# Optimization experiments

Measured on AMD Instinct MI355X. Metric: run time of the kernel, lower is better.

Reference implementation:

```python
import jax, jax.numpy as jnp
import numpy as np

B, DIM, H, W = 8, 384, 64, 64
HEADS = 8
D = DIM // HEADS          # 48
D2 = D // 2               # 24
DU = D // 3 * 2           # 32 (ratio=3)


def setup_inputs() -> dict:
    key = jax.random.key(0)
    ks = jax.random.split(key, 12)
    s = lambda k, shape, scale=0.05: jax.random.normal(k, shape, jnp.float32) * scale
    return {
        "x": jax.random.normal(ks[0], (B, DIM, H, W), jnp.float32),
        "temperature": jnp.ones((HEADS, 1, 1), jnp.float32),
        "w_qkv": s(ks[1], (3 * DIM, DIM)),          # 1x1 conv, no bias
        "w_dw": s(ks[2], (3 * DIM, 1, 3, 3)),       # depthwise 3x3, groups=3*dim
        "w_proj": s(ks[3], (DIM, HEADS)),           # project_out 1x1
        "w_attn_r": s(ks[4], (1, D)),
        "w_v_r": s(ks[5], (D2, D)),
        "w_up1": s(ks[6], (DU, D2)),
        "b_up1": jnp.zeros((DU,), jnp.float32),
        "ln_w": jnp.ones((DU, HEADS, 1), jnp.float32),
        "ln_b": jnp.zeros((DU, HEADS, 1), jnp.float32),
        "w_up2": s(ks[7], (D, DU)),
        "b_up2": jnp.zeros((D,), jnp.float32),
        "w_attn_l": s(ks[8], (D2, D)),
        "w_v_l": s(ks[9], (D2, D)),
    }


def _qkv_attn(x, temperature, w_qkv, w_dw):
    # shared: qkv 1x1 conv -> depthwise 3x3 -> split, normalize, elementwise attn+softmax
    b, c, h, w = x.shape
    qkv = jnp.einsum('bchw,oc->bohw', x, w_qkv)
    qkv = jax.lax.conv_general_dilated(
        qkv, w_dw, (1, 1), 'SAME', feature_group_count=3 * c,
        dimension_numbers=('NCHW', 'OIHW', 'NCHW'))
    q, k, v = jnp.split(qkv, 3, axis=1)
    rs = lambda t: t.reshape(b, HEADS, D, h * w)  # b (head d) h w -> b head d (hw)
    q, k, v = rs(q), rs(k), rs(v)
    qn = q / jnp.maximum(jnp.linalg.norm(q, axis=-1, keepdims=True), 1e-12)
    kn = k / jnp.maximum(jnp.linalg.norm(k, axis=-1, keepdims=True), 1e-12)
    attn = jax.nn.softmax(qn * kn * temperature, axis=-1)  # [b, head, d, s]
    return attn, v


def _forward(x, temperature, w_qkv, w_dw, w_proj, w_attn_r, w_v_r,
             w_up1, b_up1, ln_w, ln_b, w_up2, b_up2, w_attn_l, w_v_l):
    b, c, h, w = x.shape
    attn, v = _qkv_attn(x, temperature, w_qkv, w_dw)

    # ---- spatial_pool (channel gating) ----
    input_x = jnp.einsum('bhds,od->bhos', v, w_v_r)                 # conv_v_right: [b,head,d2,s]
    cm = jax.nn.softmax(jnp.einsum('bhds,d->bhs', attn, w_attn_r[0]), axis=-1)  # conv_attn_right + softmax
    ctx = jnp.einsum('bhs,bhjs->bhj', cm, input_x)                  # [b,head,d2]
    ctx = ctx.transpose(0, 2, 1)[..., None]                         # [b, d2, head, 1]
    u = jnp.einsum('bchl,oc->bohl', ctx, w_up1) + b_up1[None, :, None, None]  # [b, DU, head, 1]
    mu = u.mean(axis=(1, 2, 3), keepdims=True)
    var = u.var(axis=(1, 2, 3), keepdims=True)
    u = (u - mu) / jnp.sqrt(var + 1e-5) * ln_w[None] + ln_b[None]   # LayerNorm([DU, 8, 1])
    u = jax.nn.relu(u)
    u = jnp.einsum('bchl,oc->bohl', u, w_up2) + b_up2[None, :, None, None]    # [b, D, head, 1]
    mask_ch = jax.nn.sigmoid(u).reshape(b, c, 1, 1)                 # view(b, head*D, 1, 1)
    out_channel = x * mask_ch

    # ---- channel_pool (spatial gating) ----
    g = jnp.einsum('bhds,od->bhos', attn, w_attn_l)                 # conv_attn_left: [b,head,d2,s]
    avg = jax.nn.softmax(g.mean(axis=-1), axis=-1)                  # avg-pool over s, softmax over d2
    theta = jnp.einsum('bhds,od->bhos', v, w_v_l)                   # conv_v_left: [b,head,d2,s]
    ctx2 = jnp.einsum('bhd,bhds->bhs', avg, theta)                  # matmul: [b,head,s]
    mask_sp = jax.nn.sigmoid(ctx2).reshape(b, HEADS, h, w)
    mask_sp = jnp.einsum('bchw,oc->bohw', mask_sp, w_proj)          # project_out
    out_spatial = x * mask_sp

    return out_spatial + out_channel


def reference(x, temperature, w_qkv, w_dw, w_proj, w_attn_r, w_v_r,
              w_up1, b_up1, ln_w, ln_b, w_up2, b_up2, w_attn_l, w_v_l):
    return _forward(x, temperature, w_qkv, w_dw, w_proj, w_attn_r, w_v_r,
                    w_up1, b_up1, ln_w, ln_b, w_up2, b_up2, w_attn_l, w_v_l)
```

## Files before the change

kernel.cpp:

```cpp
#include <hip/hip_runtime.h>
#include <math.h>


#define S4096 4096
#define C384  384
#define OC    1152

typedef unsigned short bfraw;
typedef unsigned int   u32;
typedef __attribute__((ext_vector_type(8))) short bf16x8;
typedef __attribute__((ext_vector_type(4))) float f32x4;

typedef __attribute__((address_space(3))) unsigned int lds_u32;
typedef const __attribute__((address_space(1))) unsigned int glb_u32;
__device__ __forceinline__ void gll16(const void* g, void* l) {
    __builtin_amdgcn_global_load_lds((glb_u32*)g, (lds_u32*)l, 16, 0, 0);
}

__device__ __forceinline__ bfraw f2bf(float f) {
    union { float f; u32 u; } c; c.f = f;
    u32 r = c.u + 0x7FFFu + ((c.u >> 16) & 1u);
    return (bfraw)(r >> 16);
}
__device__ __forceinline__ float bf2f(bfraw u) {
    union { u32 u; float f; } c; c.u = ((u32)u) << 16;
    return c.f;
}
__device__ __forceinline__ void unpack8(uint4 v, float* f) {
    f[0] = bf2f((bfraw)(v.x & 0xffff)); f[1] = bf2f((bfraw)(v.x >> 16));
    f[2] = bf2f((bfraw)(v.y & 0xffff)); f[3] = bf2f((bfraw)(v.y >> 16));
    f[4] = bf2f((bfraw)(v.z & 0xffff)); f[5] = bf2f((bfraw)(v.z >> 16));
    f[6] = bf2f((bfraw)(v.w & 0xffff)); f[7] = bf2f((bfraw)(v.w >> 16));
}
__device__ __forceinline__ uint4 pack8(const float* f) {
    union { bfraw us[8]; uint4 q; } p;
    #pragma unroll
    for (int i = 0; i < 8; i++) p.us[i] = f2bf(f[i]);
    return p.q;
}

__device__ __forceinline__ float blk_red(float v, float* s4, bool ismax) {
    #pragma unroll
    for (int off = 32; off; off >>= 1) {
        float o = __shfl_down(v, off, 64);
        v = ismax ? fmaxf(v, o) : (v + o);
    }
    __syncthreads();
    if ((threadIdx.x & 63) == 0) s4[threadIdx.x >> 6] = v;
    __syncthreads();
    return ismax ? fmaxf(fmaxf(s4[0], s4[1]), fmaxf(s4[2], s4[3]))
                 : ((s4[0] + s4[1]) + (s4[2] + s4[3]));
}

__global__ __launch_bounds__(256) void kA_prep(
    const float* __restrict__ w_qkv, bfraw* __restrict__ wF,
    const float* __restrict__ w_attn_l, const float* __restrict__ w_v_l,
    float* __restrict__ weff) {
    if (blockIdx.x == 216) {
        __shared__ float avg[24];
        const int tid = threadIdx.x;
        if (tid < 24) {
            float a = 0.f;
            for (int d = 0; d < 48; d++) a += w_attn_l[tid * 48 + d];
            avg[tid] = a * (1.f / 4096.f);
        }
        __syncthreads();
        if (tid == 0) {
            float M = -3.402823466e+38f;
            for (int o = 0; o < 24; o++) M = fmaxf(M, avg[o]);
            float S = 0.f;
            for (int o = 0; o < 24; o++) { avg[o] = __expf(avg[o] - M); S += avg[o]; }
            float inv = 1.f / S;
            for (int o = 0; o < 24; o++) avg[o] *= inv;
        }
        __syncthreads();
        if (tid < 48) {
            float a = 0.f;
            for (int o = 0; o < 24; o++) a += avg[o] * w_v_l[o * 48 + tid];
            weff[tid] = a;
        }
        return;
    }
    const int id = blockIdx.x * 256 + threadIdx.x;
    const int ob = id / 768, rem = id % 768;
    const int c = rem / 48, kb = rem % 48;
    const float* src = w_qkv + (size_t)(ob * 16 + c) * C384 + kb * 8;
    float f[8];
    *(float4*)f       = *(const float4*)src;
    *(float4*)(f + 4) = *(const float4*)(src + 4);
    *(uint4*)&wF[((size_t)(ob * 48 + kb) * 16 + c) * 8] = pack8(f);
}

__global__ __launch_bounds__(256) void kB_tr(
    const float* __restrict__ x, bfraw* __restrict__ xF, int b0) {
    const int cb = blockIdx.x, sb = blockIdx.y, bl = blockIdx.z;
    const int c0 = cb * 16, s0 = sb * 256;
    const int tid = threadIdx.x;
    __shared__ alignas(16) bfraw lt[16][264];
    {
        const int r = tid >> 4, seg = tid & 15;
        const float* src = x + ((size_t)(b0 + bl) * C384 + c0 + r) * S4096 + s0 + seg * 16;
        float f[16];
        #pragma unroll
        for (int i = 0; i < 4; i++) *(float4*)(f + i * 4) = *(const float4*)(src + i * 4);
        *(uint4*)&lt[r][seg * 16]     = pack8(f);
        *(uint4*)&lt[r][seg * 16 + 8] = pack8(f + 8);
    }
    __syncthreads();
    const int sbl = tid >> 4, c = tid & 15;
    bfraw* xFb = xF + (size_t)bl * S4096 * C384;
    #pragma unroll
    for (int kbl = 0; kbl < 2; kbl++) {
        union { bfraw us[8]; uint4 q; } p;
        #pragma unroll
        for (int j = 0; j < 8; j++) p.us[j] = lt[kbl * 8 + j][sbl * 16 + c];
        const size_t idx = (((size_t)((s0 >> 4) + sbl) * 48) + (c0 >> 3) + kbl) * 128 + c * 8;
        *(uint4*)&xFb[idx] = p.q;
    }
}

__global__ __launch_bounds__(256) void k1_gemm(
    const bfraw* __restrict__ wF, const bfraw* __restrict__ xF,
    bfraw* __restrict__ pre, int b0) {
    __shared__ alignas(16) bfraw b_sm[2][4096];
    const int tid = threadIdx.x;
    const int wave = tid >> 6, lane = tid & 63;
    const int sT = blockIdx.x, oT = blockIdx.y, bl = blockIdx.z;
    const bfraw* xFb = xF + (size_t)bl * S4096 * C384;

    const int c0_ = tid, c1_ = tid + 256;
    const int rb0 = c0_ >> 6, oc0 = (c0_ >> 4) & 3, rw0 = c0_ & 15;
    const int rb1 = c1_ >> 6, oc1 = (c1_ >> 4) & 3, rw1 = c1_ & 15;
    const bfraw* pB0 = xFb + ((size_t)((sT * 8 + rb0) * 48 + oc0) * 16 + rw0) * 8;
    const bfraw* pB1 = xFb + ((size_t)((sT * 8 + rb1) * 48 + oc1) * 16 + rw1) * 8;

    const int wr = (wave >> 1) * 4;
    const int wc = (wave & 1) * 4;
    const int l15 = lane & 15, kq = lane >> 4;

    const bfraw* pA[4];
    #pragma unroll
    for (int m = 0; m < 4; m++)
        pA[m] = wF + (((size_t)(oT * 8 + wr + m) * 48 + kq) * 16 + l15) * 8;

    f32x4 acc[4][4];
    #pragma unroll
    for (int m = 0; m < 4; m++)
        #pragma unroll
        for (int n = 0; n < 4; n++) acc[m][n] = (f32x4){0, 0, 0, 0};

    gll16(pB0, &b_sm[0][(size_t)c0_ * 8]);
    gll16(pB1, &b_sm[0][(size_t)c1_ * 8]);
    bf16x8 a_cur[4];
    #pragma unroll
    for (int m = 0; m < 4; m++) a_cur[m] = *(const bf16x8*)(pA[m]);
    __syncthreads();

    #pragma unroll
    for (int ks = 0; ks < 12; ks++) {
        const bfraw* cb = b_sm[ks & 1];
        bf16x8 bq[4];
        #pragma unroll
        for (int n = 0; n < 4; n++)
            bq[n] = *(const bf16x8*)&cb[((wc + n) * 64 + lane) * 8];
        bf16x8 a_nxt[4];
        if (ks < 11) {
            bfraw* nb = (bfraw*)b_sm[(ks & 1) ^ 1];
            gll16(pB0 + (ks + 1) * 512, nb + (size_t)c0_ * 8);
            gll16(pB1 + (ks + 1) * 512, nb + (size_t)c1_ * 8);
            #pragma unroll
            for (int m = 0; m < 4; m++)
                a_nxt[m] = *(const bf16x8*)(pA[m] + (ks + 1) * 512);
        }
        __builtin_amdgcn_s_setprio(1);
        #pragma unroll
        for (int m = 0; m < 4; m++)
            #pragma unroll
            for (int n = 0; n < 4; n++)
                acc[m][n] = __builtin_amdgcn_mfma_f32_16x16x32_bf16(a_cur[m], bq[n], acc[m][n], 0, 0, 0);
        __builtin_amdgcn_s_setprio(0);
        if (ks < 11) {
            #pragma unroll
            for (int m = 0; m < 4; m++) a_cur[m] = a_nxt[m];
        }
        __syncthreads();
    }

    bfraw* op = pre + (size_t)bl * OC * S4096;
    const int orow0 = oT * 128 + (wave >> 1) * 64 + (lane >> 4) * 4;
    const int scol0 = sT * 128 + (wave & 1) * 64 + l15;
    #pragma unroll
    for (int m = 0; m < 4; m++)
        #pragma unroll
        for (int n = 0; n < 4; n++)
            #pragma unroll
            for (int r = 0; r < 4; r++)
                op[(size_t)(orow0 + m * 16 + r) * S4096 + scol0 + n * 16] = f2bf(acc[m][n][r]);
}

__device__ __forceinline__ void stencil8(const bfraw* plane, const float* w9,
                                         int ypad, int k7, int x0, float* acc) {
    #pragma unroll
    for (int j = 0; j < 8; j++) acc[j] = 0.f;
    #pragma unroll
    for (int dy = 0; dy < 3; dy++) {
        uint4 rv = *(const uint4*)&plane[(ypad + dy) * 64 + x0];
        float r[8]; unpack8(rv, r);
        float lft = __shfl_up(r[7], 1);
        float rgt = __shfl_down(r[0], 1);
        if (k7 == 0) lft = 0.f;
        if (k7 == 7) rgt = 0.f;
        const float w0 = w9[dy*3], w1 = w9[dy*3+1], w2 = w9[dy*3+2];
        acc[0] += w0*lft + w1*r[0] + w2*r[1];
        #pragma unroll
        for (int j = 1; j < 7; j++) acc[j] += w0*r[j-1] + w1*r[j] + w2*r[j+1];
        acc[7] += w0*r[6] + w1*r[7] + w2*rgt;
    }
}

__global__ __launch_bounds__(256) void k2f(
    const bfraw* __restrict__ pre, const float* __restrict__ w_dw,
    const float* __restrict__ temperature,
    bfraw* __restrict__ av, int b0) {
    const int idx = blockIdx.x;
    const int bl  = blockIdx.y;
    const int h   = idx / 48;
    const int tid = threadIdx.x;
    __shared__ alignas(16) bfraw pl[3][66 * 64];
    __shared__ float s4[4];

    const size_t pbase = (size_t)bl * OC * S4096;
    #pragma unroll
    for (int p = 0; p < 3; p++) {
        const bfraw* src = pre + pbase + (size_t)(idx + p * C384) * S4096;
        uint4 a = *(const uint4*)&src[tid * 16];
        uint4 b = *(const uint4*)&src[tid * 16 + 8];
        int y = tid >> 2, xq = (tid & 3) * 16;
        *(uint4*)&pl[p][(y + 1) * 64 + xq]     = a;
        *(uint4*)&pl[p][(y + 1) * 64 + xq + 8] = b;
    }
    if (tid < 64) {
        #pragma unroll
        for (int p = 0; p < 3; p++) { pl[p][tid] = 0; pl[p][65 * 64 + tid] = 0; }
    }
    float wq[9], wk[9], wv[9];
    #pragma unroll
    for (int i = 0; i < 9; i++) {
        wq[i] = w_dw[idx * 9 + i];
        wk[i] = w_dw[(idx + C384) * 9 + i];
        wv[i] = w_dw[(idx + 768) * 9 + i];
    }
    __syncthreads();

    const int sid0 = tid,        y0 = sid0 >> 3, k70 = sid0 & 7, x00 = k70 * 8;
    const int sid1 = tid + 256,  y1 = sid1 >> 3, k71 = sid1 & 7, x01 = k71 * 8;
    float qo[16], ko[16], vo[16];
    stencil8(pl[0], wq, y0, k70, x00, qo);
    stencil8(pl[0], wq, y1, k71, x01, qo + 8);
    stencil8(pl[1], wk, y0, k70, x00, ko);
    stencil8(pl[1], wk, y1, k71, x01, ko + 8);
    stencil8(pl[2], wv, y0, k70, x00, vo);
    stencil8(pl[2], wv, y1, k71, x01, vo + 8);

    float sq = 0.f, sk = 0.f;
    #pragma unroll
    for (int i = 0; i < 16; i++) { sq += qo[i] * qo[i]; sk += ko[i] * ko[i]; }
    float Sq = blk_red(sq, s4, false);
    float Sk = blk_red(sk, s4, false);
    float scale = temperature[h] /
        (fmaxf(sqrtf(Sq), 1e-12f) * fmaxf(sqrtf(Sk), 1e-12f));
    float lm = -3.402823466e+38f;
    #pragma unroll
    for (int i = 0; i < 16; i++) { qo[i] = qo[i] * ko[i] * scale; lm = fmaxf(lm, qo[i]); }
    float M = blk_red(lm, s4, true);
    float ls = 0.f;
    #pragma unroll
    for (int i = 0; i < 16; i++) { qo[i] = __expf(qo[i] - M); ls += qo[i]; }
    float Z = blk_red(ls, s4, false);
    float invZ = 1.f / Z;
    #pragma unroll
    for (int i = 0; i < 16; i++) qo[i] *= invZ;

    bfraw* adst = av + ((size_t)bl * 768 + idx) * S4096;
    bfraw* vdst = av + ((size_t)bl * 768 + 384 + idx) * S4096;
    *(uint4*)&adst[y0 * 64 + x00] = pack8(qo);
    *(uint4*)&adst[y1 * 64 + x01] = pack8(qo + 8);
    *(uint4*)&vdst[y0 * 64 + x00] = pack8(vo);
    *(uint4*)&vdst[y1 * 64 + x01] = pack8(vo + 8);
}

__global__ __launch_bounds__(256) void k4a(
    const bfraw* __restrict__ av, const float* __restrict__ w_attn_r,
    const float* __restrict__ weff,
    bfraw* __restrict__ cmraw, bfraw* __restrict__ c2raw, int b0) {
    const int h = blockIdx.x, bl = blockIdx.y, st = blockIdx.z;
    const int b = b0 + bl;
    const int tid = threadIdx.x;
    __shared__ float swr[48], swf[48];
    if (tid < 48) { swr[tid] = w_attn_r[tid]; swf[tid] = weff[tid]; }
    __syncthreads();
    const int s_off = st * 1024 + tid * 4;
    const bfraw* abase = av + ((size_t)bl * 768 + h * 48) * S4096 + s_off;
    const bfraw* vbase = abase + (size_t)384 * S4096;
    float cmr[4] = {0,0,0,0}, c2[4] = {0,0,0,0};
    for (int d = 0; d < 48; d++) {
        uint2 ua = *(const uint2*)(abase + (size_t)d * S4096);
        uint2 uv = *(const uint2*)(vbase + (size_t)d * S4096);
        const float wr = swr[d], wf = swf[d];
        cmr[0] += bf2f((bfraw)(ua.x & 0xffff)) * wr;
        cmr[1] += bf2f((bfraw)(ua.x >> 16))    * wr;
        cmr[2] += bf2f((bfraw)(ua.y & 0xffff)) * wr;
        cmr[3] += bf2f((bfraw)(ua.y >> 16))    * wr;
        c2[0]  += bf2f((bfraw)(uv.x & 0xffff)) * wf;
        c2[1]  += bf2f((bfraw)(uv.x >> 16))    * wf;
        c2[2]  += bf2f((bfraw)(uv.y & 0xffff)) * wf;
        c2[3]  += bf2f((bfraw)(uv.y >> 16))    * wf;
    }
    const size_t o = ((size_t)(b * 8 + h)) * S4096 + s_off;
    union { bfraw us[4]; uint2 q; } pa, pb;
    #pragma unroll
    for (int j = 0; j < 4; j++) { pa.us[j] = f2bf(cmr[j]); pb.us[j] = f2bf(c2[j]); }
    *(uint2*)(cmraw + o) = pa.q;
    *(uint2*)(c2raw + o) = pb.q;
}

__global__ __launch_bounds__(256) void k4b(
    const bfraw* __restrict__ cmraw, const bfraw* __restrict__ c2raw,
    bfraw* __restrict__ cmb, bfraw* __restrict__ msp, int b0) {
    const int h = blockIdx.x, bl = blockIdx.y, b = b0 + bl;
    const int tid = threadIdx.x;
    __shared__ float s4[4];
    const size_t base = ((size_t)(b * 8 + h)) * S4096 + tid * 16;
    float v[16];
    { uint4 a = *(const uint4*)(cmraw + base), c = *(const uint4*)(cmraw + base + 8);
      unpack8(a, v); unpack8(c, v + 8); }
    float lm = -3.402823466e+38f;
    #pragma unroll
    for (int i = 0; i < 16; i++) lm = fmaxf(lm, v[i]);
    float M = blk_red(lm, s4, true);
    float ls = 0.f;
    #pragma unroll
    for (int i = 0; i < 16; i++) { v[i] = __expf(v[i] - M); ls += v[i]; }
    float Z = blk_red(ls, s4, false);
    float inv = 1.f / Z;
    #pragma unroll
    for (int i = 0; i < 16; i++) v[i] *= inv;
    *(uint4*)(cmb + base)     = pack8(v);
    *(uint4*)(cmb + base + 8) = pack8(v + 8);
    float sg[16];
    { uint4 a = *(const uint4*)(c2raw + base), c = *(const uint4*)(c2raw + base + 8);
      unpack8(a, sg); unpack8(c, sg + 8); }
    #pragma unroll
    for (int i = 0; i < 16; i++) sg[i] = 1.f / (1.f + __expf(-sg[i]));
    *(uint4*)(msp + base)     = pack8(sg);
    *(uint4*)(msp + base + 8) = pack8(sg + 8);
}

__global__ __launch_bounds__(256) void k5_vc(
    const bfraw* __restrict__ av, const bfraw* __restrict__ cmb,
    float* __restrict__ vc, int b0) {
    const int idx = blockIdx.x;
    const int bl = blockIdx.y, b = b0 + bl;
    const int h = idx / 48;
    const int tid = threadIdx.x;
    const bfraw* vr = av + ((size_t)bl * 768 + 384 + idx) * S4096 + tid * 16;
    const bfraw* cr = cmb + ((size_t)(b * 8 + h)) * S4096 + tid * 16;
    float vv[16], cc[16];
    { uint4 a = *(const uint4*)vr, c = *(const uint4*)(vr + 8); unpack8(a, vv); unpack8(c, vv + 8); }
    { uint4 a = *(const uint4*)cr, c = *(const uint4*)(cr + 8); unpack8(a, cc); unpack8(c, cc + 8); }
    float a = 0.f;
    #pragma unroll
    for (int i = 0; i < 16; i++) a += vv[i] * cc[i];
    __shared__ float s4[4];
    float S = blk_red(a, s4, false);
    if (tid == 0) vc[b * C384 + idx] = S;
}

__global__ __launch_bounds__(256) void k6_gate(
    const float* __restrict__ vc, const float* __restrict__ w_v_r,
    const float* __restrict__ w_up1, const float* __restrict__ b_up1,
    const float* __restrict__ ln_w, const float* __restrict__ ln_b,
    const float* __restrict__ w_up2, const float* __restrict__ b_up2,
    float* __restrict__ mch, int b0) {
    const int b = b0 + blockIdx.x;
    const int tid = threadIdx.x;
    __shared__ float s_vc[384], s_ctx[192], s_u[256], s4[4];
    for (int i = tid; i < 384; i += 256) s_vc[i] = vc[b * C384 + i];
    __syncthreads();
    if (tid < 192) {
        int hh = tid / 24, o = tid % 24;
        float a = 0.f;
        for (int d = 0; d < 48; d++) a += w_v_r[o * 48 + d] * s_vc[hh * 48 + d];
        s_ctx[hh * 24 + o] = a;
    }
    __syncthreads();
    float uval;
    {
        int o = tid >> 3, hh = tid & 7;
        float a = b_up1[o];
        for (int c = 0; c < 24; c++) a += w_up1[o * 24 + c] * s_ctx[hh * 24 + c];
        uval = a;
    }
    float mu  = blk_red(uval, s4, false) * (1.f / 256.f);
    float dv  = uval - mu;
    float var = blk_red(dv * dv, s4, false) * (1.f / 256.f);
    float un  = dv * rsqrtf(var + 1e-5f) * ln_w[tid] + ln_b[tid];
    s_u[tid] = fmaxf(un, 0.f);
    __syncthreads();
    for (int t = tid; t < 384; t += 256) {
        int o2 = t >> 3, hh = t & 7;
        float a = b_up2[o2];
        for (int o = 0; o < 32; o++) a += w_up2[o2 * 32 + o] * s_u[o * 8 + hh];
        mch[b * C384 + t] = 1.f / (1.f + __expf(-a));
    }
}

__global__ __launch_bounds__(256) void k7_out(
    const float* __restrict__ x, const float* __restrict__ w_proj,
    const float* __restrict__ mch, const bfraw* __restrict__ msp,
    float* __restrict__ out, int b0) {
    const int st = blockIdx.x, cg = blockIdx.y, bl = blockIdx.z;
    const int b = b0 + bl;
    const int tid = threadIdx.x;
    const int s0 = st * 256, c0 = cg * 48;
    __shared__ float s_msp[8][256];
    __shared__ float s_mch[48];
    __shared__ float s_wp[48][8];
    for (int i = tid; i < 2048; i += 256) {
        int hh = i >> 8, ss = i & 255;
        s_msp[hh][ss] = bf2f(msp[((size_t)(b * 8 + hh)) * S4096 + s0 + ss]);
    }
    if (tid < 48) s_mch[tid] = mch[b * C384 + c0 + tid];
    for (int i = tid; i < 384; i += 256)
        s_wp[i >> 3][i & 7] = w_proj[(size_t)(c0 + (i >> 3)) * 8 + (i & 7)];
    __syncthreads();

    const int cl = tid >> 6;
    const int s4i = (tid & 63) * 4;
    float4 m[8];
    #pragma unroll
    for (int hh = 0; hh < 8; hh++) m[hh] = *(const float4*)&s_msp[hh][s4i];

    #pragma unroll 4
    for (int j = 0; j < 12; j++) {
        const int cloc = j * 4 + cl;
        const int c = c0 + cloc;
        const float base = s_mch[cloc];
        float4 a = {base, base, base, base};
        #pragma unroll
        for (int hh = 0; hh < 8; hh++) {
            const float wp = s_wp[cloc][hh];
            a.x += wp * m[hh].x; a.y += wp * m[hh].y;
            a.z += wp * m[hh].z; a.w += wp * m[hh].w;
        }
        const size_t o = ((size_t)b * C384 + c) * S4096 + s0 + s4i;
        float4 xv = *(const float4*)(x + o);
        a.x *= xv.x; a.y *= xv.y; a.z *= xv.z; a.w *= xv.w;
        *(float4*)(out + o) = a;
    }
}

extern "C" void kernel_launch(void* const* d_in, const int* in_sizes, int n_in,
                              void* d_out, int out_size, void* d_ws, size_t ws_size,
                              hipStream_t stream) {
    const float* x        = (const float*)d_in[0];
    const float* temp     = (const float*)d_in[1];
    const float* w_qkv    = (const float*)d_in[2];
    const float* w_dw     = (const float*)d_in[3];
    const float* w_proj   = (const float*)d_in[4];
    const float* w_attn_r = (const float*)d_in[5];
    const float* w_v_r    = (const float*)d_in[6];
    const float* w_up1    = (const float*)d_in[7];
    const float* b_up1    = (const float*)d_in[8];
    const float* ln_w     = (const float*)d_in[9];
    const float* ln_b     = (const float*)d_in[10];
    const float* w_up2    = (const float*)d_in[11];
    const float* b_up2    = (const float*)d_in[12];
    const float* w_attn_l = (const float*)d_in[13];
    const float* w_v_l    = (const float*)d_in[14];
    float* out = (float*)d_out;
    char* ws = (char*)d_ws;

    size_t off = 0;
    auto alloc = [&](size_t bytes) {
        size_t o = off; off = (off + bytes + 255) & ~(size_t)255; return o;
    };
    bfraw* cmraw = (bfraw*)(ws + alloc((size_t)64 * S4096 * 2));
    bfraw* c2raw = (bfraw*)(ws + alloc((size_t)64 * S4096 * 2));
    bfraw* cmb   = (bfraw*)(ws + alloc((size_t)64 * S4096 * 2));
    bfraw* msp   = (bfraw*)(ws + alloc((size_t)64 * S4096 * 2));
    float* vc    = (float*)(ws + alloc(3072 * 4));
    float* mch   = (float*)(ws + alloc(3072 * 4));
    float* weff  = (float*)(ws + alloc(256));
    bfraw* wF    = (bfraw*)(ws + alloc((size_t)55296 * 16));
    const size_t big_xF  = (size_t)S4096 * C384 * 2;
    const size_t big_pre = (size_t)OC * S4096 * 2;
    const size_t big_av  = (size_t)768 * S4096 * 2;
    int nb = (ws_size >= off + 8 * (big_xF + big_pre + big_av)) ? 8 : 1;
    bfraw* xF  = (bfraw*)(ws + alloc((size_t)nb * big_xF));
    bfraw* pre = (bfraw*)(ws + alloc((size_t)nb * big_pre));
    bfraw* av  = (bfraw*)(ws + alloc((size_t)nb * big_av));

    kA_prep<<<217, 256, 0, stream>>>(w_qkv, wF, w_attn_l, w_v_l, weff);
    for (int b0 = 0; b0 < 8; b0 += nb) {
        kB_tr<<<dim3(24, 16, nb), 256, 0, stream>>>(x, xF, b0);
        k1_gemm<<<dim3(32, 9, nb), 256, 0, stream>>>(wF, xF, pre, b0);
        k2f<<<dim3(384, nb), 256, 0, stream>>>(pre, w_dw, temp, av, b0);
        k4a<<<dim3(8, nb, 4), 256, 0, stream>>>(av, w_attn_r, weff, cmraw, c2raw, b0);
        k4b<<<dim3(8, nb), 256, 0, stream>>>(cmraw, c2raw, cmb, msp, b0);
        k5_vc<<<dim3(384, nb), 256, 0, stream>>>(av, cmb, vc, b0);
        k6_gate<<<dim3(nb), 256, 0, stream>>>(vc, w_v_r, w_up1, b_up1,
                                              ln_w, ln_b, w_up2, b_up2, mch, b0);
        k7_out<<<dim3(16, 8, nb), 256, 0, stream>>>(x, w_proj, mch, msp, out, b0);
    }
}
```

Measured before the change: 126.4 us.

## Fuse gating projections, softmax, sigmoid and v-context reduction into one kernel

New measurement: 153.3 us. 21.2% more time.

```diff
diff --git a/kernel.cpp b/kernel.cpp
--- a/kernel.cpp
+++ b/kernel.cpp
@@ -289,91 +289,69 @@
     *(uint4*)&vdst[y1 * 64 + x01] = pack8(vo + 8);
 }
 
-__global__ __launch_bounds__(256) void k4a(
+__global__ __launch_bounds__(256) void k45(
     const bfraw* __restrict__ av, const float* __restrict__ w_attn_r,
     const float* __restrict__ weff,
-    bfraw* __restrict__ cmraw, bfraw* __restrict__ c2raw, int b0) {
-    const int h = blockIdx.x, bl = blockIdx.y, st = blockIdx.z;
-    const int b = b0 + bl;
-    const int tid = threadIdx.x;
-    __shared__ float swr[48], swf[48];
+    bfraw* __restrict__ msp, float* __restrict__ vc, int b0) {
+    const int h = blockIdx.x, bl = blockIdx.y, b = b0 + bl;
+    const int tid = threadIdx.x;
+    __shared__ float swr[48], swf[48], s4[4];
     if (tid < 48) { swr[tid] = w_attn_r[tid]; swf[tid] = weff[tid]; }
     __syncthreads();
-    const int s_off = st * 1024 + tid * 4;
-    const bfraw* abase = av + ((size_t)bl * 768 + h * 48) * S4096 + s_off;
+    const bfraw* abase = av + ((size_t)bl * 768 + h * 48) * S4096 + tid * 16;
     const bfraw* vbase = abase + (size_t)384 * S4096;
-    float cmr[4] = {0,0,0,0}, c2[4] = {0,0,0,0};
+
+    float cmr[16], c2[16];
+    #pragma unroll
+    for (int i = 0; i < 16; i++) { cmr[i] = 0.f; c2[i] = 0.f; }
     for (int d = 0; d < 48; d++) {
-        uint2 ua = *(const uint2*)(abase + (size_t)d * S4096);
-        uint2 uv = *(const uint2*)(vbase + (size_t)d * S4096);
+        float af[16], vf[16];
+        { uint4 u0 = *(const uint4*)(abase + (size_t)d * S4096);
+          uint4 u1 = *(const uint4*)(abase + (size_t)d * S4096 + 8);
+          unpack8(u0, af); unpack8(u1, af + 8); }
+        { uint4 u0 = *(const uint4*)(vbase + (size_t)d * S4096);
+          uint4 u1 = *(const uint4*)(vbase + (size_t)d * S4096 + 8);
+          unpack8(u0, vf); unpack8(u1, vf + 8); }
         const float wr = swr[d], wf = swf[d];
-        cmr[0] += bf2f((bfraw)(ua.x & 0xffff)) * wr;
-        cmr[1] += bf2f((bfraw)(ua.x >> 16))    * wr;
-        cmr[2] += bf2f((bfraw)(ua.y & 0xffff)) * wr;
-        cmr[3] += bf2f((bfraw)(ua.y >> 16))    * wr;
-        c2[0]  += bf2f((bfraw)(uv.x & 0xffff)) * wf;
-        c2[1]  += bf2f((bfraw)(uv.x >> 16))    * wf;
-        c2[2]  += bf2f((bfraw)(uv.y & 0xffff)) * wf;
-        c2[3]  += bf2f((bfraw)(uv.y >> 16))    * wf;
-    }
-    const size_t o = ((size_t)(b * 8 + h)) * S4096 + s_off;
-    union { bfraw us[4]; uint2 q; } pa, pb;
-    #pragma unroll
-    for (int j = 0; j < 4; j++) { pa.us[j] = f2bf(cmr[j]); pb.us[j] = f2bf(c2[j]); }
-    *(uint2*)(cmraw + o) = pa.q;
-    *(uint2*)(c2raw + o) = pb.q;
-}
-
-__global__ __launch_bounds__(256) void k4b(
-    const bfraw* __restrict__ cmraw, const bfraw* __restrict__ c2raw,
-    bfraw* __restrict__ cmb, bfraw* __restrict__ msp, int b0) {
-    const int h = blockIdx.x, bl = blockIdx.y, b = b0 + bl;
-    const int tid = threadIdx.x;
-    __shared__ float s4[4];
-    const size_t base = ((size_t)(b * 8 + h)) * S4096 + tid * 16;
-    float v[16];
-    { uint4 a = *(const uint4*)(cmraw + base), c = *(const uint4*)(cmraw + base + 8);
-      unpack8(a, v); unpack8(c, v + 8); }
+        #pragma unroll
+        for (int i = 0; i < 16; i++) { cmr[i] += af[i] * wr; c2[i] += vf[i] * wf; }
+    }
+
     float lm = -3.402823466e+38f;
     #pragma unroll
-    for (int i = 0; i < 16; i++) lm = fmaxf(lm, v[i]);
+    for (int i = 0; i < 16; i++) lm = fmaxf(lm, cmr[i]);
     float M = blk_red(lm, s4, true);
     float ls = 0.f;
     #pragma unroll
-    for (int i = 0; i < 16; i++) { v[i] = __expf(v[i] - M); ls += v[i]; }
+    for (int i = 0; i < 16; i++) { cmr[i] = __expf(cmr[i] - M); ls += cmr[i]; }
     float Z = blk_red(ls, s4, false);
     float inv = 1.f / Z;
     #pragma unroll
-    for (int i = 0; i < 16; i++) v[i] *= inv;
-    *(uint4*)(cmb + base)     = pack8(v);
-    *(uint4*)(cmb + base + 8) = pack8(v + 8);
+    for (int i = 0; i < 16; i++) cmr[i] *= inv;
+
+    const size_t mbase = ((size_t)(b * 8 + h)) * S4096 + tid * 16;
     float sg[16];
-    { uint4 a = *(const uint4*)(c2raw + base), c = *(const uint4*)(c2raw + base + 8);
-      unpack8(a, sg); unpack8(c, sg + 8); }
-    #pragma unroll
-    for (int i = 0; i < 16; i++) sg[i] = 1.f / (1.f + __expf(-sg[i]));
-    *(uint4*)(msp + base)     = pack8(sg);
-    *(uint4*)(msp + base + 8) = pack8(sg + 8);
-}
-
-__global__ __launch_bounds__(256) void k5_vc(
-    const bfraw* __restrict__ av, const bfraw* __restrict__ cmb,
-    float* __restrict__ vc, int b0) {
-    const int idx = blockIdx.x;
-    const int bl = blockIdx.y, b = b0 + bl;
-    const int h = idx / 48;
-    const int tid = threadIdx.x;
-    const bfraw* vr = av + ((size_t)bl * 768 + 384 + idx) * S4096 + tid * 16;
-    const bfraw* cr = cmb + ((size_t)(b * 8 + h)) * S4096 + tid * 16;
-    float vv[16], cc[16];
-    { uint4 a = *(const uint4*)vr, c = *(const uint4*)(vr + 8); unpack8(a, vv); unpack8(c, vv + 8); }
-    { uint4 a = *(const uint4*)cr, c = *(const uint4*)(cr + 8); unpack8(a, cc); unpack8(c, cc + 8); }
-    float a = 0.f;
-    #pragma unroll
-    for (int i = 0; i < 16; i++) a += vv[i] * cc[i];
-    __shared__ float s4[4];
-    float S = blk_red(a, s4, false);
-    if (tid == 0) vc[b * C384 + idx] = S;
+    #pragma unroll
+    for (int i = 0; i < 16; i++) sg[i] = 1.f / (1.f + __expf(-c2[i]));
+    *(uint4*)(msp + mbase)     = pack8(sg);
+    *(uint4*)(msp + mbase + 8) = pack8(sg + 8);
+
+    float* vcb = vc + b * C384 + h * 48;
+    uint4 p0 = *(const uint4*)(vbase);
+    uint4 p1 = *(const uint4*)(vbase + 8);
+    for (int d = 0; d < 48; d++) {
+        float vf[16];
+        unpack8(p0, vf); unpack8(p1, vf + 8);
+        if (d < 47) {
+            p0 = *(const uint4*)(vbase + (size_t)(d + 1) * S4096);
+            p1 = *(const uint4*)(vbase + (size_t)(d + 1) * S4096 + 8);
+        }
+        float a = 0.f;
+        #pragma unroll
+        for (int i = 0; i < 16; i++) a += cmr[i] * vf[i];
+        float S = blk_red(a, s4, false);
+        if (tid == 0) vcb[d] = S;
+    }
 }
 
 __global__ __launch_bounds__(256) void k6_gate(
@@ -485,9 +463,6 @@
     auto alloc = [&](size_t bytes) {
         size_t o = off; off = (off + bytes + 255) & ~(size_t)255; return o;
     };
-    bfraw* cmraw = (bfraw*)(ws + alloc((size_t)64 * S4096 * 2));
-    bfraw* c2raw = (bfraw*)(ws + alloc((size_t)64 * S4096 * 2));
-    bfraw* cmb   = (bfraw*)(ws + alloc((size_t)64 * S4096 * 2));
     bfraw* msp   = (bfraw*)(ws + alloc((size_t)64 * S4096 * 2));
     float* vc    = (float*)(ws + alloc(3072 * 4));
     float* mch   = (float*)(ws + alloc(3072 * 4));
@@ -506,9 +481,7 @@
         kB_tr<<<dim3(24, 16, nb), 256, 0, stream>>>(x, xF, b0);
         k1_gemm<<<dim3(32, 9, nb), 256, 0, stream>>>(wF, xF, pre, b0);
         k2f<<<dim3(384, nb), 256, 0, stream>>>(pre, w_dw, temp, av, b0);
-        k4a<<<dim3(8, nb, 4), 256, 0, stream>>>(av, w_attn_r, weff, cmraw, c2raw, b0);
-        k4b<<<dim3(8, nb), 256, 0, stream>>>(cmraw, c2raw, cmb, msp, b0);
-        k5_vc<<<dim3(384, nb), 256, 0, stream>>>(av, cmb, vc, b0);
+        k45<<<dim3(8, nb), 256, 0, stream>>>(av, w_attn_r, weff, msp, vc, b0);
         k6_gate<<<dim3(nb), 256, 0, stream>>>(vc, w_v_r, w_up1, b_up1,
                                               ln_w, ln_b, w_up2, b_up2, mch, b0);
         k7_out<<<dim3(16, 8, nb), 256, 0, stream>>>(x, w_proj, mch, msp, out, b0);
```
